# Kernel tuning notes

Measured on AMD Instinct MI355X. Metric: run time of the kernel, lower is better.

The kernel has to match this reference:

```python
import jax, jax.numpy as jnp
import numpy as np

B, N, K, D, L = 8, 1024, 16, 256, 3  # batch, max_node_num, neighbor fan-in, g_hidden_dim, layers


def setup_inputs() -> dict:
    key = jax.random.key(0)
    ks = jax.random.split(key, 14)
    f32 = jnp.float32
    scale = 1.0 / np.sqrt(D).astype(np.float32)
    randn = lambda k, s: jax.random.normal(k, s, dtype=f32)
    lens = jax.random.randint(ks[12], (B,), N // 2, N + 1)
    node_mask = (jnp.arange(N)[None, :] < lens[:, None]).astype(f32)
    return {
        "h0": randn(ks[0], (B, N, D)),
        "c0": randn(ks[1], (B, N, D)),
        "x_in": randn(ks[2], (B, N, D)),
        "x_out": randn(ks[3], (B, N, D)),
        "W_in": randn(ks[4], (4, D, D)) * scale,   # gates stacked: [i, o, f, cell]
        "U_in": randn(ks[5], (4, D, D)) * scale,
        "W_out": randn(ks[6], (4, D, D)) * scale,
        "U_out": randn(ks[7], (4, D, D)) * scale,
        "b": jnp.zeros((4, D), dtype=f32),
        "in_mask": jax.random.randint(ks[8], (B, N, K), 0, 2).astype(f32),
        "out_mask": jax.random.randint(ks[9], (B, N, K), 0, 2).astype(f32),
        "node_mask": node_mask,
        "in_nodes": jax.random.randint(ks[10], (B, N, K), 0, N, dtype=jnp.int32),
        "out_nodes": jax.random.randint(ks[11], (B, N, K), 0, N, dtype=jnp.int32),
        "num_layers": L,
    }


def _gather_agg(h, idx, nb_mask, node_mask):
    # h: [B,N,D], idx: [B,N,K] -> masked sum of neighbor hidden states [B,N,D]
    nb = jax.vmap(lambda hb, ib: hb[ib])(h, idx)           # [B,N,K,D]
    agg = jnp.einsum('bnkd,bnk->bnd', nb, nb_mask)
    return agg * node_mask[..., None]


def reference(h0, c0, x_in, x_out, W_in, U_in, W_out, U_out, b,
              in_mask, out_mask, node_mask, in_nodes, out_nodes, num_layers):
    h, c = h0, c0
    nm = node_mask[..., None]
    for _ in range(num_layers):
        h_in = _gather_agg(h, in_nodes, in_mask, node_mask)
        h_out = _gather_agg(h, out_nodes, out_mask, node_mask)
        # pre-activation for all 4 gates at once: [4,B,N,D]
        pre = (jnp.einsum('bnd,gde->gbne', x_in, W_in)
               + jnp.einsum('bnd,gde->gbne', h_in, U_in)
               + jnp.einsum('bnd,gde->gbne', x_out, W_out)
               + jnp.einsum('bnd,gde->gbne', h_out, U_out)
               + b[:, None, None, :])
        i_g = jax.nn.sigmoid(pre[0])
        o_g = jax.nn.sigmoid(pre[1])
        f_g = jax.nn.sigmoid(pre[2])
        g = jnp.tanh(pre[3])
        c = (f_g * c + i_g * g) * nm
        h = o_g * jnp.tanh(c) * nm
    return h
```

## Files before the change

### kernel.cpp

```cpp
#include <hip/hip_runtime.h>
#include <hip/hip_bf16.h>
#include <cstdint>
#include <cstddef>

typedef __hip_bfloat16 bf16;
typedef _Float16 f16;
typedef __attribute__((ext_vector_type(4))) float f32x4;
typedef __attribute__((ext_vector_type(8))) _Float16 f16x8;
typedef __attribute__((ext_vector_type(4))) _Float16 f16x4;

#define BB 8
#define NN 1024
#define KK 16
#define DD 256
#define MM (BB * NN)
#define GW 1024
#define NLAYER 3

__device__ __forceinline__ float ldf(const void* p, size_t i, int isf32) {
  return isf32 ? ((const float*)p)[i] : __bfloat162float(((const bf16*)p)[i]);
}

__device__ __forceinline__ void gload_lds16(const void* g, void* l) {
  __builtin_amdgcn_global_load_lds(
      (const __attribute__((address_space(1))) unsigned int*)g,
      (__attribute__((address_space(3))) unsigned int*)l, 16, 0, 0);
}

__global__ void detect_dtype(const unsigned short* __restrict__ w, int* __restrict__ flag) {
  __shared__ int cnt;
  if (threadIdx.x == 0) cnt = 0;
  __syncthreads();
  int sane = 0;
  for (int i = threadIdx.x; i < 512; i += 256) {
    unsigned short b = w[2 * i];
    int e = (b >> 7) & 0xFF;
    if ((e >= 105 && e <= 130) || (b & 0x7FFF) == 0) sane++;
  }
  atomicAdd(&cnt, sane);
  __syncthreads();
  if (threadIdx.x == 0) flag[0] = (cnt > 256) ? 0 : 1;
}

__global__ void prep(const void* __restrict__ bvec, const void* __restrict__ node_mask,
                     const void* __restrict__ in_mask, const void* __restrict__ out_mask,
                     const void* __restrict__ h0, const void* __restrict__ c0,
                     const void* __restrict__ x_in, const void* __restrict__ x_out,
                     float* __restrict__ biasI, float* __restrict__ nmF,
                     float* __restrict__ inmF, float* __restrict__ outmF,
                     f16* __restrict__ h, f16* __restrict__ c,
                     f16* __restrict__ Ax, const int* __restrict__ flag) {
  int isf32 = flag[0];
  size_t t = (size_t)blockIdx.x * 256 + threadIdx.x;
  const size_t S0 = 1024;
  const size_t S1 = S0 + MM;
  const size_t S2 = S1 + (size_t)MM * KK;
  const size_t S3 = S2 + (size_t)MM * KK;
  const size_t S4 = S3 + (size_t)MM * DD;
  const size_t S5 = S4 + (size_t)MM * DD;
  if (t < S0) {
    size_t e = t >> 2, g = t & 3;
    biasI[t] = ldf(bvec, g * 256 + e, isf32);
  } else if (t < S1) {
    nmF[t - S0] = ldf(node_mask, t - S0, isf32);
  } else if (t < S2) {
    inmF[t - S1] = ldf(in_mask, t - S1, isf32);
  } else if (t < S3) {
    outmF[t - S2] = ldf(out_mask, t - S2, isf32);
  } else if (t < S4) {
    size_t i = t - S3;
    h[i] = (f16)ldf(h0, i, isf32);
    c[i] = (f16)ldf(c0, i, isf32);
  } else if (t < S5) {
    size_t i = t - S4;
    size_t m = i >> 8, d = i & 255;
    Ax[m * 512 + d]       = (f16)ldf(x_in, m * DD + d, isf32);
    Ax[m * 512 + 256 + d] = (f16)ldf(x_out, m * DD + d, isf32);
  }
}

__global__ void transpose_w(const void* __restrict__ W_in, const void* __restrict__ W_out,
                            const void* __restrict__ U_in, const void* __restrict__ U_out,
                            f16* __restrict__ WT, f16* __restrict__ UT,
                            const int* __restrict__ flag) {
  int isf32 = flag[0];
  int z = blockIdx.z; int g = z & 3; int which = z >> 2;
  const void* src = (which == 0) ? W_in : (which == 1) ? W_out : (which == 2) ? U_in : U_out;
  f16* dst = (which < 2) ? WT : UT;
  int colofs = (which & 1) ? DD : 0;
  size_t gbase = (size_t)g * DD * DD;
  __shared__ float tile[64][65];
  int tx = threadIdx.x & 63, ty = threadIdx.x >> 6;
  int d0 = blockIdx.x * 64, e0 = blockIdx.y * 64;
#pragma unroll
  for (int r = 0; r < 64; r += 4)
    tile[ty + r][tx] = ldf(src, gbase + (size_t)(d0 + ty + r) * DD + e0 + tx, isf32);
  __syncthreads();
#pragma unroll
  for (int r = 0; r < 64; r += 4)
    dst[(size_t)(4 * (e0 + ty + r) + g) * 512 + colofs + d0 + tx] = (f16)tile[tx][ty + r];
}

__global__ void gather_agg(const f16* __restrict__ h,
                           const int* __restrict__ in_nodes, const int* __restrict__ out_nodes,
                           const float* __restrict__ in_mask, const float* __restrict__ out_mask,
                           const float* __restrict__ node_mask,
                           f16* __restrict__ A) {
  int m = blockIdx.x;
  int t = threadIdx.x;
  int dir = t >> 6;
  int d4 = (t & 63) * 4;
  __shared__ int   s_idx[32];
  __shared__ float s_w[32];
  if (t < 32) {
    int dd = t >> 4, k = t & 15;
    const int*   nodes = dd ? out_nodes : in_nodes;
    const float* mask  = dd ? out_mask  : in_mask;
    s_idx[t] = nodes[(size_t)m * KK + k];
    s_w[t]   = mask[(size_t)m * KK + k];
  }
  __syncthreads();
  const f16* hb = h + (size_t)(m >> 10) * NN * DD;
  f32x4 acc = {};
#pragma unroll
  for (int k = 0; k < KK; k++) {
    int   idx = s_idx[dir * 16 + k];
    float wv  = s_w[dir * 16 + k];
    f16x4 v = *(const f16x4*)(hb + (size_t)idx * DD + d4);
#pragma unroll
    for (int q = 0; q < 4; q++) acc[q] += wv * (float)v[q];
  }
  float nm = node_mask[m];
  f16x4 o;
#pragma unroll
  for (int q = 0; q < 4; q++) o[q] = (f16)(acc[q] * nm);
  *(f16x4*)(A + (size_t)m * 512 + dir * DD + d4) = o;
}

#define BM 64
#define BN 128
#define BK 64
#define KTOT 512
__global__ __launch_bounds__(256, 4)
void gemm_fused(const f16* __restrict__ A, const f16* __restrict__ Bt,
                const f16* __restrict__ pre_x, const float* __restrict__ biasI,
                int mode,
                f16* __restrict__ cbuf, f16* __restrict__ hbuf,
                const float* __restrict__ node_mask,
                void* __restrict__ outp, int last, const int* __restrict__ flag,
                f16* __restrict__ prex_out) {
  __shared__ char smem[24576];
  f16*   As   = (f16*)smem;
  f16*   Bs   = (f16*)(smem + 8192);
  float* tile = (float*)smem;

  int t = threadIdx.x;
  int w = t >> 6, lane = t & 63;
  int row16 = lane & 15, kgrp = lane >> 4;
  int mBase = blockIdx.x * BM, nBase = blockIdx.y * BN;

  int aoff[2][4], boff[2][2];
#pragma unroll
  for (int sub = 0; sub < 2; sub++) {
    int ch = ((sub * 4 + kgrp) ^ (row16 & 7)) * 8;
#pragma unroll
    for (int i = 0; i < 4; i++)
      aoff[sub][i] = (row16 + 16 * i) * 64 + ch;
#pragma unroll
    for (int j = 0; j < 2; j++)
      boff[sub][j] = (w * 32 + 16 * j + row16) * 64 + ch;
  }

  int srow = t >> 3;
  int scol = ((t & 7) ^ (srow & 7)) * 8;
  const f16* ga0 = A  + (size_t)(mBase + srow) * 512 + scol;
  const f16* gb0 = Bt + (size_t)(nBase + srow) * 512 + scol;

  f32x4 acc[4][2] = {};

  for (int kt = 0; kt < KTOT; kt += BK) {
    const f16* ga = ga0 + kt;
    const f16* gb = gb0 + kt;
#pragma unroll
    for (int q = 0; q < 2; q++)
      gload_lds16(ga + (size_t)(32 * q) * 512, As + q * 2048 + t * 8);
#pragma unroll
    for (int q = 0; q < 4; q++)
      gload_lds16(gb + (size_t)(32 * q) * 512, Bs + q * 2048 + t * 8);
    __syncthreads();

#pragma unroll
    for (int sub = 0; sub < 2; sub++) {
      f16x8 af[4], bfr[2];
#pragma unroll
      for (int i = 0; i < 4; i++) af[i] = *(const f16x8*)(As + aoff[sub][i]);
#pragma unroll
      for (int j = 0; j < 2; j++) bfr[j] = *(const f16x8*)(Bs + boff[sub][j]);
#pragma unroll
      for (int i = 0; i < 4; i++)
#pragma unroll
        for (int j = 0; j < 2; j++)
          acc[i][j] = __builtin_amdgcn_mfma_f32_16x16x32_f16(af[i], bfr[j], acc[i][j], 0, 0, 0);
    }
    __syncthreads();
  }

  if (mode == 0) {
#pragma unroll
    for (int i = 0; i < 4; i++)
#pragma unroll
      for (int j = 0; j < 2; j++) {
        int gn = nBase + w * 32 + 16 * j + row16;
        float bv = biasI[gn];
#pragma unroll
        for (int r = 0; r < 4; r++) {
          int gm = mBase + 16 * i + kgrp * 4 + r;
          prex_out[(size_t)gm * GW + gn] = (f16)(acc[i][j][r] + bv);
        }
      }
    return;
  }

  int isf32 = flag[0];
#pragma unroll
  for (int p = 0; p < 2; p++) {
    __syncthreads();
    if ((w >> 1) == p) {
#pragma unroll
      for (int i = 0; i < 4; i++)
#pragma unroll
        for (int j = 0; j < 2; j++) {
          int cl = (w & 1) * 32 + 16 * j + row16;
#pragma unroll
          for (int r = 0; r < 4; r++) {
            int rr = 16 * i + 4 * kgrp + r;
            int ch = (cl >> 2) ^ (rr & 7);
            tile[rr * 64 + ch * 4 + (cl & 3)] = acc[i][j][r];
          }
        }
    }
    __syncthreads();

    int el = t & 15;
    int nb = nBase + 64 * p;
    int eb = nb >> 2;
#pragma unroll
    for (int rep = 0; rep < 4; rep++) {
      int ml = rep * 16 + (t >> 4);
      int gm = mBase + ml;
      f32x4 vals = *(const f32x4*)(tile + ml * 64 + ((el ^ (ml & 7))) * 4);
      f16x4 pxh = *(const f16x4*)(pre_x + (size_t)gm * GW + nb + el * 4);
      float nm = node_mask[gm];
      size_t ci = (size_t)gm * DD + eb + el;
      float cold = (float)cbuf[ci];
      float p_i = vals[0] + (float)pxh[0];
      float p_o = vals[1] + (float)pxh[1];
      float p_f = vals[2] + (float)pxh[2];
      float p_g = vals[3] + (float)pxh[3];
      float ig = 1.f / (1.f + expf(-p_i));
      float og = 1.f / (1.f + expf(-p_o));
      float fg = 1.f / (1.f + expf(-p_f));
      float gg = tanhf(p_g);
      float cn = (fg * cold + ig * gg) * nm;
      float hn = og * tanhf(cn) * nm;
      cbuf[ci] = (f16)cn;
      hbuf[ci] = (f16)hn;
      if (last) {
        if (isf32) ((float*)outp)[ci] = hn;
        else       ((bf16*)outp)[ci] = __float2bfloat16(hn);
      }
    }
  }
}

extern "C" void kernel_launch(void* const* d_in, const int* in_sizes, int n_in,
                              void* d_out, int out_size, void* d_ws, size_t ws_size,
                              hipStream_t stream) {
  const void* h0      = d_in[0];
  const void* c0      = d_in[1];
  const void* x_in    = d_in[2];
  const void* x_out   = d_in[3];
  const void* W_in    = d_in[4];
  const void* U_in    = d_in[5];
  const void* W_out   = d_in[6];
  const void* U_out   = d_in[7];
  const void* bvec    = d_in[8];
  const void* in_mask = d_in[9];
  const void* out_mask= d_in[10];
  const void* node_mask = d_in[11];
  const int*  in_nodes  = (const int*)d_in[12];
  const int*  out_nodes = (const int*)d_in[13];

  char* ws = (char*)d_ws;
  int*   flag  = (int*)ws;
  f16*   h_cur = (f16*)(ws + 256);
  f16*   c_cur = h_cur + (size_t)MM * DD;
  f16*   A_x   = c_cur + (size_t)MM * DD;
  f16*   A_h   = A_x + (size_t)MM * 512;
  f16*   pre_x = A_h + (size_t)MM * 512;
  f16*   WT    = pre_x + (size_t)MM * GW;
  f16*   UT    = WT + (size_t)1024 * 512;
  float* biasI = (float*)(UT + (size_t)1024 * 512);
  float* nmF   = biasI + 1024;
  float* inmF  = nmF + MM;
  float* outmF = inmF + (size_t)MM * KK;

  detect_dtype<<<1, 256, 0, stream>>>((const unsigned short*)W_in, flag);

  {
    size_t total = 1024 + MM + 2 * (size_t)MM * KK + 2 * (size_t)MM * DD;
    prep<<<(int)((total + 255) / 256), 256, 0, stream>>>(
        bvec, node_mask, in_mask, out_mask, h0, c0, x_in, x_out,
        biasI, nmF, inmF, outmF, h_cur, c_cur, A_x, flag);
  }
  transpose_w<<<dim3(4, 4, 16), 256, 0, stream>>>(W_in, W_out, U_in, U_out, WT, UT, flag);

  gemm_fused<<<dim3(MM / BM, GW / BN), 256, 0, stream>>>(
      A_x, WT, nullptr, biasI, 0, nullptr, nullptr, nullptr, nullptr, 0, flag, pre_x);

  for (int l = 0; l < NLAYER; l++) {
    gather_agg<<<MM, 128, 0, stream>>>(h_cur, in_nodes, out_nodes,
                                       inmF, outmF, nmF, A_h);
    gemm_fused<<<dim3(MM / BM, GW / BN), 256, 0, stream>>>(
        A_h, UT, pre_x, nullptr, 1, c_cur, h_cur, nmF,
        d_out, l == NLAYER - 1, flag, nullptr);
  }
}
```

Measured before the change: 229.2 us.

## Fold input projection into per-layer GEMM with concatenated K and widen gather

Removes the one-time x-projection GEMM and its pre_x buffer. Instead it concatenates [x_in, x_out, h_in, h_out] into a single 1024-wide A matrix and the matching weights into one B, so each layer's GEMM computes all four terms and adds the bias in the epilogue. This drops the pre_x write and the per-layer reads, but doubles the GEMM K dimension every layer, recomputing the x projection three times. The gather kernel now processes four nodes per block, one wave each, distributing indices with shuffles and using 16-byte loads.

```diff
diff --git a/kernel.cpp b/kernel.cpp
--- a/kernel.cpp
+++ b/kernel.cpp
@@ -7,7 +7,6 @@
 typedef _Float16 f16;
 typedef __attribute__((ext_vector_type(4))) float f32x4;
 typedef __attribute__((ext_vector_type(8))) _Float16 f16x8;
-typedef __attribute__((ext_vector_type(4))) _Float16 f16x4;
 
 #define BB 8
 #define NN 1024
@@ -49,7 +48,7 @@
                      float* __restrict__ biasI, float* __restrict__ nmF,
                      float* __restrict__ inmF, float* __restrict__ outmF,
                      f16* __restrict__ h, f16* __restrict__ c,
-                     f16* __restrict__ Ax, const int* __restrict__ flag) {
+                     f16* __restrict__ A, const int* __restrict__ flag) {
   int isf32 = flag[0];
   size_t t = (size_t)blockIdx.x * 256 + threadIdx.x;
   const size_t S0 = 1024;
@@ -74,20 +73,18 @@
   } else if (t < S5) {
     size_t i = t - S4;
     size_t m = i >> 8, d = i & 255;
-    Ax[m * 512 + d]       = (f16)ldf(x_in, m * DD + d, isf32);
-    Ax[m * 512 + 256 + d] = (f16)ldf(x_out, m * DD + d, isf32);
+    A[m * 1024 + d]       = (f16)ldf(x_in, m * DD + d, isf32);
+    A[m * 1024 + 256 + d] = (f16)ldf(x_out, m * DD + d, isf32);
   }
 }
 
 __global__ void transpose_w(const void* __restrict__ W_in, const void* __restrict__ W_out,
                             const void* __restrict__ U_in, const void* __restrict__ U_out,
-                            f16* __restrict__ WT, f16* __restrict__ UT,
-                            const int* __restrict__ flag) {
+                            f16* __restrict__ BT, const int* __restrict__ flag) {
   int isf32 = flag[0];
   int z = blockIdx.z; int g = z & 3; int which = z >> 2;
   const void* src = (which == 0) ? W_in : (which == 1) ? W_out : (which == 2) ? U_in : U_out;
-  f16* dst = (which < 2) ? WT : UT;
-  int colofs = (which & 1) ? DD : 0;
+  int colofs = which * 256;
   size_t gbase = (size_t)g * DD * DD;
   __shared__ float tile[64][65];
   int tx = threadIdx.x & 63, ty = threadIdx.x >> 6;
@@ -98,7 +95,7 @@
   __syncthreads();
 #pragma unroll
   for (int r = 0; r < 64; r += 4)
-    dst[(size_t)(4 * (e0 + ty + r) + g) * 512 + colofs + d0 + tx] = (f16)tile[tx][ty + r];
+    BT[(size_t)(4 * (e0 + ty + r) + g) * 1024 + colofs + d0 + tx] = (f16)tile[tx][ty + r];
 }
 
 __global__ void gather_agg(const f16* __restrict__ h,
@@ -106,49 +103,43 @@
                            const float* __restrict__ in_mask, const float* __restrict__ out_mask,
                            const float* __restrict__ node_mask,
                            f16* __restrict__ A) {
-  int m = blockIdx.x;
-  int t = threadIdx.x;
-  int dir = t >> 6;
-  int d4 = (t & 63) * 4;
-  __shared__ int   s_idx[32];
-  __shared__ float s_w[32];
-  if (t < 32) {
-    int dd = t >> 4, k = t & 15;
-    const int*   nodes = dd ? out_nodes : in_nodes;
-    const float* mask  = dd ? out_mask  : in_mask;
-    s_idx[t] = nodes[(size_t)m * KK + k];
-    s_w[t]   = mask[(size_t)m * KK + k];
-  }
-  __syncthreads();
+  int wave = threadIdx.x >> 6;
+  int lane = threadIdx.x & 63;
+  int m = blockIdx.x * 4 + wave;
+  int l5 = lane & 31, dir = lane >> 5;
+  int myidx = 0; float mymask = 0.f;
+  if (lane < 16)      { myidx = in_nodes[(size_t)m * KK + lane];
+                        mymask = in_mask[(size_t)m * KK + lane]; }
+  else if (lane < 32) { myidx = out_nodes[(size_t)m * KK + lane - 16];
+                        mymask = out_mask[(size_t)m * KK + lane - 16]; }
   const f16* hb = h + (size_t)(m >> 10) * NN * DD;
-  f32x4 acc = {};
+  float acc[8] = {};
 #pragma unroll
   for (int k = 0; k < KK; k++) {
-    int   idx = s_idx[dir * 16 + k];
-    float wv  = s_w[dir * 16 + k];
-    f16x4 v = *(const f16x4*)(hb + (size_t)idx * DD + d4);
-#pragma unroll
-    for (int q = 0; q < 4; q++) acc[q] += wv * (float)v[q];
+    int src = dir * 16 + k;
+    int idxk = __shfl(myidx, src);
+    float wk = __shfl(mymask, src);
+    f16x8 v = *(const f16x8*)(hb + (size_t)idxk * DD + l5 * 8);
+#pragma unroll
+    for (int q = 0; q < 8; q++) acc[q] += wk * (float)v[q];
   }
   float nm = node_mask[m];
-  f16x4 o;
-#pragma unroll
-  for (int q = 0; q < 4; q++) o[q] = (f16)(acc[q] * nm);
-  *(f16x4*)(A + (size_t)m * 512 + dir * DD + d4) = o;
+  f16x8 o;
+#pragma unroll
+  for (int q = 0; q < 8; q++) o[q] = (f16)(acc[q] * nm);
+  *(f16x8*)(A + (size_t)m * 1024 + 512 + dir * 256 + l5 * 8) = o;
 }
 
 #define BM 64
 #define BN 128
 #define BK 64
-#define KTOT 512
+#define KTOT 1024
 __global__ __launch_bounds__(256, 4)
 void gemm_fused(const f16* __restrict__ A, const f16* __restrict__ Bt,
-                const f16* __restrict__ pre_x, const float* __restrict__ biasI,
-                int mode,
+                const float* __restrict__ biasI,
                 f16* __restrict__ cbuf, f16* __restrict__ hbuf,
                 const float* __restrict__ node_mask,
-                void* __restrict__ outp, int last, const int* __restrict__ flag,
-                f16* __restrict__ prex_out) {
+                void* __restrict__ outp, int last, const int* __restrict__ flag) {
   __shared__ char smem[24576];
   f16*   As   = (f16*)smem;
   f16*   Bs   = (f16*)(smem + 8192);
@@ -173,8 +164,8 @@
 
   int srow = t >> 3;
   int scol = ((t & 7) ^ (srow & 7)) * 8;
-  const f16* ga0 = A  + (size_t)(mBase + srow) * 512 + scol;
-  const f16* gb0 = Bt + (size_t)(nBase + srow) * 512 + scol;
+  const f16* ga0 = A  + (size_t)(mBase + srow) * 1024 + scol;
+  const f16* gb0 = Bt + (size_t)(nBase + srow) * 1024 + scol;
 
   f32x4 acc[4][2] = {};
 
@@ -183,10 +174,10 @@
     const f16* gb = gb0 + kt;
 #pragma unroll
     for (int q = 0; q < 2; q++)
-      gload_lds16(ga + (size_t)(32 * q) * 512, As + q * 2048 + t * 8);
+      gload_lds16(ga + (size_t)(32 * q) * 1024, As + q * 2048 + t * 8);
 #pragma unroll
     for (int q = 0; q < 4; q++)
-      gload_lds16(gb + (size_t)(32 * q) * 512, Bs + q * 2048 + t * 8);
+      gload_lds16(gb + (size_t)(32 * q) * 1024, Bs + q * 2048 + t * 8);
     __syncthreads();
 
 #pragma unroll
@@ -203,22 +194,6 @@
           acc[i][j] = __builtin_amdgcn_mfma_f32_16x16x32_f16(af[i], bfr[j], acc[i][j], 0, 0, 0);
     }
     __syncthreads();
-  }
-
-  if (mode == 0) {
-#pragma unroll
-    for (int i = 0; i < 4; i++)
-#pragma unroll
-      for (int j = 0; j < 2; j++) {
-        int gn = nBase + w * 32 + 16 * j + row16;
-        float bv = biasI[gn];
-#pragma unroll
-        for (int r = 0; r < 4; r++) {
-          int gm = mBase + 16 * i + kgrp * 4 + r;
-          prex_out[(size_t)gm * GW + gn] = (f16)(acc[i][j][r] + bv);
-        }
-      }
-    return;
   }
 
   int isf32 = flag[0];
@@ -244,19 +219,19 @@
     int el = t & 15;
     int nb = nBase + 64 * p;
     int eb = nb >> 2;
+    f32x4 bv4 = *(const f32x4*)(biasI + nb + el * 4);
 #pragma unroll
     for (int rep = 0; rep < 4; rep++) {
       int ml = rep * 16 + (t >> 4);
       int gm = mBase + ml;
       f32x4 vals = *(const f32x4*)(tile + ml * 64 + ((el ^ (ml & 7))) * 4);
-      f16x4 pxh = *(const f16x4*)(pre_x + (size_t)gm * GW + nb + el * 4);
       float nm = node_mask[gm];
       size_t ci = (size_t)gm * DD + eb + el;
       float cold = (float)cbuf[ci];
-      float p_i = vals[0] + (float)pxh[0];
-      float p_o = vals[1] + (float)pxh[1];
-      float p_f = vals[2] + (float)pxh[2];
-      float p_g = vals[3] + (float)pxh[3];
+      float p_i = vals[0] + bv4[0];
+      float p_o = vals[1] + bv4[1];
+      float p_f = vals[2] + bv4[2];
+      float p_g = vals[3] + bv4[3];
       float ig = 1.f / (1.f + expf(-p_i));
       float og = 1.f / (1.f + expf(-p_o));
       float fg = 1.f / (1.f + expf(-p_f));
@@ -295,12 +270,9 @@
   int*   flag  = (int*)ws;
   f16*   h_cur = (f16*)(ws + 256);
   f16*   c_cur = h_cur + (size_t)MM * DD;
-  f16*   A_x   = c_cur + (size_t)MM * DD;
-  f16*   A_h   = A_x + (size_t)MM * 512;
-  f16*   pre_x = A_h + (size_t)MM * 512;
-  f16*   WT    = pre_x + (size_t)MM * GW;
-  f16*   UT    = WT + (size_t)1024 * 512;
-  float* biasI = (float*)(UT + (size_t)1024 * 512);
+  f16*   A_buf = c_cur + (size_t)MM * DD;
+  f16*   BT    = A_buf + (size_t)MM * 1024;
+  float* biasI = (float*)(BT + (size_t)1024 * 1024);
   float* nmF   = biasI + 1024;
   float* inmF  = nmF + MM;
   float* outmF = inmF + (size_t)MM * KK;
@@ -311,18 +283,15 @@
     size_t total = 1024 + MM + 2 * (size_t)MM * KK + 2 * (size_t)MM * DD;
     prep<<<(int)((total + 255) / 256), 256, 0, stream>>>(
         bvec, node_mask, in_mask, out_mask, h0, c0, x_in, x_out,
-        biasI, nmF, inmF, outmF, h_cur, c_cur, A_x, flag);
-  }
-  transpose_w<<<dim3(4, 4, 16), 256, 0, stream>>>(W_in, W_out, U_in, U_out, WT, UT, flag);
-
-  gemm_fused<<<dim3(MM / BM, GW / BN), 256, 0, stream>>>(
-      A_x, WT, nullptr, biasI, 0, nullptr, nullptr, nullptr, nullptr, 0, flag, pre_x);
+        biasI, nmF, inmF, outmF, h_cur, c_cur, A_buf, flag);
+  }
+  transpose_w<<<dim3(4, 4, 16), 256, 0, stream>>>(W_in, W_out, U_in, U_out, BT, flag);
 
   for (int l = 0; l < NLAYER; l++) {
-    gather_agg<<<MM, 128, 0, stream>>>(h_cur, in_nodes, out_nodes,
-                                       inmF, outmF, nmF, A_h);
+    gather_agg<<<MM / 4, 256, 0, stream>>>(h_cur, in_nodes, out_nodes,
+                                           inmF, outmF, nmF, A_buf);
     gemm_fused<<<dim3(MM / BM, GW / BN), 256, 0, stream>>>(
-        A_h, UT, pre_x, nullptr, 1, c_cur, h_cur, nmF,
-        d_out, l == NLAYER - 1, flag, nullptr);
-  }
-}
+        A_buf, BT, biasI, c_cur, h_cur, nmF,
+        d_out, l == NLAYER - 1, flag);
+  }
+}
```

New measurement: 231.6 us. No clear change (+1.0%).
